# Kernel optimization log

Hardware: AMD Instinct MI355X
Metric: run time of the kernel (lower is better)

The kernel has to match this reference:

```python
import jax, jax.numpy as jnp
import numpy as np

B = 4
N_TOTAL = 40000
N_SRC0, N_DST0, E0 = 30000, 15000, 360000
N_DST1, E1 = 7500, 180000
D_IN, OUT = 64, 32
H1, C1 = 8, 8
H2, C2 = 1, OUT
NEG_SLOPE = 0.2


def setup_inputs() -> dict:
    key = jax.random.key(0)
    ks = jax.random.split(key, 16)
    inp = {
        'x': jax.random.normal(ks[0], (B, N_TOTAL, D_IN), dtype=jnp.float32),
        'n_id0': jax.random.randint(ks[1], (N_SRC0,), 0, N_SRC0),
        'res_n_id0': jax.random.randint(ks[2], (N_DST0,), 0, N_SRC0),
        'edge_src0': jax.random.randint(ks[3], (E0,), 0, N_SRC0),
        'edge_dst0': jax.random.randint(ks[4], (E0,), 0, N_DST0),
        'res_n_id1': jax.random.randint(ks[5], (N_DST1,), 0, N_DST0),
        'edge_src1': jax.random.randint(ks[6], (E1,), 0, N_DST0),
        'edge_dst1': jax.random.randint(ks[7], (E1,), 0, N_DST1),
        # GATConv params (Glorot-ish scale)
        'W1': jax.random.normal(ks[8], (D_IN, H1 * C1), dtype=jnp.float32) / np.sqrt(D_IN),
        'att_src1': jax.random.normal(ks[9], (H1, C1), dtype=jnp.float32) / np.sqrt(C1),
        'att_dst1': jax.random.normal(ks[10], (H1, C1), dtype=jnp.float32) / np.sqrt(C1),
        'b1': jnp.zeros((H1 * C1,), dtype=jnp.float32),
        'W2': jax.random.normal(ks[11], (H1 * C1, H2 * C2), dtype=jnp.float32) / np.sqrt(H1 * C1),
        'att_src2': jax.random.normal(ks[12], (H2, C2), dtype=jnp.float32) / np.sqrt(C2),
        'att_dst2': jax.random.normal(ks[13], (H2, C2), dtype=jnp.float32) / np.sqrt(C2),
        'b2': jnp.zeros((H2 * C2,), dtype=jnp.float32),
    }
    return inp


def gat_conv(x_src, x_dst, src, dst, W, a_src, a_dst, bias, n_dst, H, C):
    """Bipartite PyG-style GATConv (concat=True, eval mode, no self-loops)."""
    b = x_src.shape[0]
    hs = (x_src @ W).reshape(b, -1, H, C)            # [B, Ns, H, C]
    hd = (x_dst @ W).reshape(b, -1, H, C)            # [B, Nd, H, C]
    es = jnp.einsum('bnhc,hc->bnh', hs, a_src)       # [B, Ns, H]
    ed = jnp.einsum('bnhc,hc->bnh', hd, a_dst)       # [B, Nd, H]
    e = jax.nn.leaky_relu(es[:, src] + ed[:, dst], NEG_SLOPE)  # [B, E, H]
    eT = jnp.swapaxes(e, 0, 1)                       # [E, B, H] (segment over axis 0)
    m = jax.ops.segment_max(eT, dst, num_segments=n_dst)
    p = jnp.exp(eT - m[dst])
    den = jax.ops.segment_sum(p, dst, num_segments=n_dst)
    alpha = p / den[dst]                             # [E, B, H]
    msg = alpha[..., None] * jnp.swapaxes(hs[:, src], 0, 1)    # [E, B, H, C]
    out = jax.ops.segment_sum(msg, dst, num_segments=n_dst)    # [Nd, B, H, C]
    out = jnp.swapaxes(out, 0, 1).reshape(b, n_dst, H * C)
    return out + bias


def reference(x, n_id0, res_n_id0, edge_src0, edge_dst0, res_n_id1, edge_src1,
              edge_dst1, W1, att_src1, att_dst1, b1, W2, att_src2, att_dst2, b2):
    xt = x[:, n_id0, :]                                        # [B, N_SRC0, D_IN]
    h = gat_conv(xt, xt[:, res_n_id0, :], edge_src0, edge_dst0,
                 W1, att_src1, att_dst1, b1, N_DST0, H1, C1)
    h = jax.nn.elu(h)                                          # dropout = identity (eval)
    out = gat_conv(h, h[:, res_n_id1, :], edge_src1, edge_dst1,
                   W2, att_src2, att_dst2, b2, N_DST1, H2, C2)
    return out                                                 # [B, N_DST1, OUT]
```

## Files before the change

### kernel.cpp

```cpp
#include <hip/hip_runtime.h>

#define NB 4
#define NT 40000
#define NS0 30000
#define ND0 15000
#define NE0 360000
#define ND1 7500
#define NE1 180000
#define NEG 0.2f

#define CAP 64
#define K1B ((NB*NS0)/64)
#define SB4 ((NE0 + NE1 + 1023)/1024)

typedef __attribute__((ext_vector_type(8))) short bf8;
typedef __attribute__((ext_vector_type(4))) float f4;

__device__ __forceinline__ unsigned short f2bf(float f) {
    unsigned u = __float_as_uint(f);
    u += 0x7FFF + ((u >> 16) & 1);
    return (unsigned short)(u >> 16);
}
__device__ __forceinline__ float bf_lo(unsigned u) { return __uint_as_float(u << 16); }
__device__ __forceinline__ float bf_hi(unsigned u) { return __uint_as_float(u & 0xFFFF0000u); }

__global__ __launch_bounds__(256) void kA_gemm_scat(
        const float* __restrict__ x, const int* __restrict__ n_id0,
        const float* __restrict__ W1, const float* __restrict__ a_src,
        const float* __restrict__ a_dst,
        unsigned short* __restrict__ ht1b, float* __restrict__ es1, float* __restrict__ ed1,
        const int* __restrict__ esrc0, const int* __restrict__ edst0,
        const int* __restrict__ esrc1, const int* __restrict__ edst1,
        int* __restrict__ cur0, int* __restrict__ cur1,
        int* __restrict__ srcsort0, int* __restrict__ srcsort1) {
    __shared__ unsigned short xtb[64*72];
    __shared__ unsigned short wtb[64*72];
    __shared__ float asl[64], adl[64];
    if (blockIdx.x < SB4) {
        int base = blockIdx.x * 1024 + threadIdx.x;
        #pragma unroll
        for (int p = 0; p < 4; ++p) {
            int t = base + p * 256;
            if (t < NE0) {
                int d = edst0[t];
                int pos = atomicAdd(&cur0[d], 1);
                if (pos < CAP) srcsort0[d*CAP + pos] = esrc0[t];
            } else if (t < NE0 + NE1) {
                int e = t - NE0;
                int d = edst1[e];
                int pos = atomicAdd(&cur1[d], 1);
                if (pos < CAP) srcsort1[d*CAP + pos] = esrc1[e];
            }
        }
        return;
    }
    int bid = blockIdx.x - SB4;
    int t = threadIdx.x;
    {
        int k = t >> 2, nb = (t & 3) * 16;
        const float* wrow = &W1[k*64 + nb];
        #pragma unroll
        for (int j = 0; j < 16; j += 4) {
            float4 v = *(const float4*)&wrow[j];
            wtb[(nb+j+0)*72 + k] = f2bf(v.x);
            wtb[(nb+j+1)*72 + k] = f2bf(v.y);
            wtb[(nb+j+2)*72 + k] = f2bf(v.z);
            wtb[(nb+j+3)*72 + k] = f2bf(v.w);
        }
    }
    if (t < 64) { asl[t] = a_src[t]; adl[t] = a_dst[t]; }
    {
        int rr = t & 63;
        int q4 = t >> 6;
        int row_s = bid * 64 + rr;
        int bs = row_s / NS0;
        int ns = row_s - bs * NS0;
        const float* xrow = x + ((size_t)(bs * NT + n_id0[ns])) * 64;
        #pragma unroll
        for (int j = 0; j < 4; ++j) {
            int k = q4 * 16 + j * 4;
            float4 v = *(const float4*)&xrow[k];
            ushort4 u;
            u.x = f2bf(v.x); u.y = f2bf(v.y); u.z = f2bf(v.z); u.w = f2bf(v.w);
            *(ushort4*)&xtb[rr*72 + k] = u;
        }
    }
    __syncthreads();
    int w = t >> 6, lane = t & 63, quad = lane >> 4, cl = lane & 15;
    int arow = 16*w + cl;
    bf8 a0 = *(const bf8*)&xtb[arow*72 + quad*8];
    bf8 a1 = *(const bf8*)&xtb[arow*72 + 32 + quad*8];
    f4 acc[4];
    #pragma unroll
    for (int sub = 0; sub < 4; ++sub) {
        int n = sub*16 + cl;
        bf8 b0 = *(const bf8*)&wtb[n*72 + quad*8];
        bf8 b1 = *(const bf8*)&wtb[n*72 + 32 + quad*8];
        f4 c = {0.f, 0.f, 0.f, 0.f};
        c = __builtin_amdgcn_mfma_f32_16x16x32_bf16(a0, b0, c, 0, 0, 0);
        c = __builtin_amdgcn_mfma_f32_16x16x32_bf16(a1, b1, c, 0, 0, 0);
        acc[sub] = c;
    }
    int rbase = bid*64 + 16*w + quad*4;
    #pragma unroll
    for (int sub = 0; sub < 4; ++sub)
        #pragma unroll
        for (int r = 0; r < 4; ++r)
            ht1b[(size_t)(rbase + r)*64 + sub*16 + cl] = f2bf(acc[sub][r]);
    #pragma unroll
    for (int r = 0; r < 4; ++r) {
        #pragma unroll
        for (int sub = 0; sub < 4; ++sub) {
            int col = sub*16 + cl;
            float ps = acc[sub][r] * asl[col];
            float pd = acc[sub][r] * adl[col];
            ps += __shfl_xor(ps, 1); ps += __shfl_xor(ps, 2); ps += __shfl_xor(ps, 4);
            pd += __shfl_xor(pd, 1); pd += __shfl_xor(pd, 2); pd += __shfl_xor(pd, 4);
            if ((cl & 7) == 0) {
                int h = sub*2 + (cl >> 3);
                es1[(rbase + r)*8 + h] = ps;
                ed1[(rbase + r)*8 + h] = pd;
            }
        }
    }
}

__global__ __launch_bounds__(256) void k3_agg1_node2(
        const int* __restrict__ srcsort0, const int* __restrict__ cur0,
        const int* __restrict__ res0,
        const float* __restrict__ es1, const float* __restrict__ ed1,
        const unsigned short* __restrict__ ht1b, const float* __restrict__ b1,
        const float* __restrict__ W2, const float* __restrict__ a_src2,
        const float* __restrict__ a_dst2,
        float* __restrict__ ht2, float* __restrict__ es2, float* __restrict__ ed2) {
    __shared__ float W2l[64*32];
    __shared__ float as2[32], ad2[32];
    __shared__ float hsh[4][64];
    int t = threadIdx.x;
    for (int i = t; i < 512; i += 256)
        *(float4*)&W2l[i*4] = *(const float4*)&W2[i*4];
    if (t < 32) { as2[t] = a_src2[t]; ad2[t] = a_dst2[t]; }
    __syncthreads();
    int xcd = blockIdx.x & 7;
    int b = xcd >> 1;
    int chunk = (blockIdx.x >> 3) * 2 + (xcd & 1);
    int wv = t >> 6;
    int d = chunk * 4 + wv;
    int lane = t & 63;
    int grp = lane >> 3;
    int c = lane & 7;
    int dn = res0[d];
    float edv = ed1[(b*NS0 + dn)*8 + c];
    int start = d * CAP;
    int cnt = cur0[d];
    const float* esb = es1 + (size_t)b*NS0*8;
    const unsigned short* htb = ht1b + (size_t)b*NS0*64;
    float acc[8] = {};
    float wsum = 0.f;
    int i = grp;
    bool v0 = i      < cnt, v1 = i + 8  < cnt,
         v2 = i + 16 < cnt, v3 = i + 24 < cnt;
    int s0 = v0 ? srcsort0[start + i]      : 0;
    int s1 = v1 ? srcsort0[start + i + 8]  : 0;
    int s2 = v2 ? srcsort0[start + i + 16] : 0;
    int s3 = v3 ? srcsort0[start + i + 24] : 0;
    for (;;) {
        float e0 = esb[s0*8 + c], e1 = esb[s1*8 + c];
        float e2 = esb[s2*8 + c], e3 = esb[s3*8 + c];
        uint4 h0 = *(const uint4*)&htb[(size_t)s0*64 + c*8];
        uint4 h1 = *(const uint4*)&htb[(size_t)s1*64 + c*8];
        uint4 h2 = *(const uint4*)&htb[(size_t)s2*64 + c*8];
        uint4 h3 = *(const uint4*)&htb[(size_t)s3*64 + c*8];
        int ni = i + 32;
        bool nv0 = ni      < cnt, nv1 = ni + 8  < cnt,
             nv2 = ni + 16 < cnt, nv3 = ni + 24 < cnt;
        int t0 = nv0 ? srcsort0[start + ni]      : 0;
        int t1 = nv1 ? srcsort0[start + ni + 8]  : 0;
        int t2 = nv2 ? srcsort0[start + ni + 16] : 0;
        int t3 = nv3 ? srcsort0[start + ni + 24] : 0;
        e0 += edv; e1 += edv; e2 += edv; e3 += edv;
        e0 = e0 > 0.f ? e0 : NEG * e0;
        e1 = e1 > 0.f ? e1 : NEG * e1;
        e2 = e2 > 0.f ? e2 : NEG * e2;
        e3 = e3 > 0.f ? e3 : NEG * e3;
        float w0 = v0 ? __expf(e0) : 0.f;
        float w1 = v1 ? __expf(e1) : 0.f;
        float w2 = v2 ? __expf(e2) : 0.f;
        float w3 = v3 ? __expf(e3) : 0.f;
        acc[0] = fmaf(w0, bf_lo(h0.x), acc[0]); acc[1] = fmaf(w0, bf_hi(h0.x), acc[1]);
        acc[2] = fmaf(w0, bf_lo(h0.y), acc[2]); acc[3] = fmaf(w0, bf_hi(h0.y), acc[3]);
        acc[4] = fmaf(w0, bf_lo(h0.z), acc[4]); acc[5] = fmaf(w0, bf_hi(h0.z), acc[5]);
        acc[6] = fmaf(w0, bf_lo(h0.w), acc[6]); acc[7] = fmaf(w0, bf_hi(h0.w), acc[7]);
        acc[0] = fmaf(w1, bf_lo(h1.x), acc[0]); acc[1] = fmaf(w1, bf_hi(h1.x), acc[1]);
        acc[2] = fmaf(w1, bf_lo(h1.y), acc[2]); acc[3] = fmaf(w1, bf_hi(h1.y), acc[3]);
        acc[4] = fmaf(w1, bf_lo(h1.z), acc[4]); acc[5] = fmaf(w1, bf_hi(h1.z), acc[5]);
        acc[6] = fmaf(w1, bf_lo(h1.w), acc[6]); acc[7] = fmaf(w1, bf_hi(h1.w), acc[7]);
        acc[0] = fmaf(w2, bf_lo(h2.x), acc[0]); acc[1] = fmaf(w2, bf_hi(h2.x), acc[1]);
        acc[2] = fmaf(w2, bf_lo(h2.y), acc[2]); acc[3] = fmaf(w2, bf_hi(h2.y), acc[3]);
        acc[4] = fmaf(w2, bf_lo(h2.z), acc[4]); acc[5] = fmaf(w2, bf_hi(h2.z), acc[5]);
        acc[6] = fmaf(w2, bf_lo(h2.w), acc[6]); acc[7] = fmaf(w2, bf_hi(h2.w), acc[7]);
        acc[0] = fmaf(w3, bf_lo(h3.x), acc[0]); acc[1] = fmaf(w3, bf_hi(h3.x), acc[1]);
        acc[2] = fmaf(w3, bf_lo(h3.y), acc[2]); acc[3] = fmaf(w3, bf_hi(h3.y), acc[3]);
        acc[4] = fmaf(w3, bf_lo(h3.z), acc[4]); acc[5] = fmaf(w3, bf_hi(h3.z), acc[5]);
        acc[6] = fmaf(w3, bf_lo(h3.w), acc[6]); acc[7] = fmaf(w3, bf_hi(h3.w), acc[7]);
        wsum += (w0 + w1) + (w2 + w3);
        i = ni; s0 = t0; s1 = t1; s2 = t2; s3 = t3;
        v0 = nv0; v1 = nv1; v2 = nv2; v3 = nv3;
        if (i >= cnt) break;
    }
    #pragma unroll
    for (int j = 0; j < 8; ++j) {
        acc[j] += __shfl_xor(acc[j], 8);
        acc[j] += __shfl_xor(acc[j], 16);
        acc[j] += __shfl_xor(acc[j], 32);
    }
    wsum += __shfl_xor(wsum, 8); wsum += __shfl_xor(wsum, 16); wsum += __shfl_xor(wsum, 32);
    if (grp == 0) {
        float inv = cnt > 0 ? 1.f / wsum : 0.f;
        float4 b_lo = *(const float4*)&b1[c*8];
        float4 b_hi = *(const float4*)&b1[c*8 + 4];
        float o[8];
        o[0] = acc[0]*inv + b_lo.x; o[1] = acc[1]*inv + b_lo.y;
        o[2] = acc[2]*inv + b_lo.z; o[3] = acc[3]*inv + b_lo.w;
        o[4] = acc[4]*inv + b_hi.x; o[5] = acc[5]*inv + b_hi.y;
        o[6] = acc[6]*inv + b_hi.z; o[7] = acc[7]*inv + b_hi.w;
        #pragma unroll
        for (int j = 0; j < 8; ++j) o[j] = o[j] > 0.f ? o[j] : __expf(o[j]) - 1.f;
        float* hrow = &hsh[wv][c*8];
        *(float4*)&hrow[0] = make_float4(o[0], o[1], o[2], o[3]);
        *(float4*)&hrow[4] = make_float4(o[4], o[5], o[6], o[7]);
    }
    int c2 = lane & 31, half = lane >> 5;
    float acc2 = 0.f;
    #pragma unroll
    for (int k = 0; k < 32; ++k)
        acc2 = fmaf(hsh[wv][half*32 + k], W2l[(half*32 + k)*32 + c2], acc2);
    acc2 += __shfl_xor(acc2, 32);
    float ps = acc2 * as2[c2];
    float pd = acc2 * ad2[c2];
    ps += __shfl_xor(ps, 1); ps += __shfl_xor(ps, 2); ps += __shfl_xor(ps, 4);
    ps += __shfl_xor(ps, 8); ps += __shfl_xor(ps, 16);
    pd += __shfl_xor(pd, 1); pd += __shfl_xor(pd, 2); pd += __shfl_xor(pd, 4);
    pd += __shfl_xor(pd, 8); pd += __shfl_xor(pd, 16);
    int row = b*ND0 + d;
    if (half == 0) ht2[(size_t)row*32 + c2] = acc2;
    if (lane == 0) { es2[row] = ps; ed2[row] = pd; }
}

__global__ __launch_bounds__(256) void k7_agg2(
        const int* __restrict__ srcsort1, const int* __restrict__ cur1,
        const int* __restrict__ res1,
        const float* __restrict__ es2, const float* __restrict__ ed2,
        const float* __restrict__ ht2, const float* __restrict__ b2,
        float* __restrict__ outp) {
    int xcd = blockIdx.x & 7;
    int b = xcd >> 1;
    int chunk = (blockIdx.x >> 3) * 2 + (xcd & 1);
    if (chunk >= ND1/4) return;
    int d = chunk * 4 + (threadIdx.x >> 6);
    int lane = threadIdx.x & 63;
    int grp = lane >> 3;
    int c = lane & 7;
    int dn = res1[d];
    float edv = ed2[b*ND0 + dn];
    int start = d * CAP;
    int cnt = cur1[d];
    const float* esb = es2 + (size_t)b*ND0;
    const float* htb = ht2 + (size_t)b*ND0*32;
    float ax = 0.f, ay = 0.f, az = 0.f, aw = 0.f, wsum = 0.f;
    int i = grp;
    bool v0 = i      < cnt, v1 = i + 8  < cnt,
         v2 = i + 16 < cnt, v3 = i + 24 < cnt;
    int s0 = v0 ? srcsort1[start + i]      : 0;
    int s1 = v1 ? srcsort1[start + i + 8]  : 0;
    int s2 = v2 ? srcsort1[start + i + 16] : 0;
    int s3 = v3 ? srcsort1[start + i + 24] : 0;
    for (;;) {
        float lg0 = esb[s0], lg1 = esb[s1], lg2 = esb[s2], lg3 = esb[s3];
        float4 h0 = *(const float4*)&htb[(size_t)s0*32 + c*4];
        float4 h1 = *(const float4*)&htb[(size_t)s1*32 + c*4];
        float4 h2 = *(const float4*)&htb[(size_t)s2*32 + c*4];
        float4 h3 = *(const float4*)&htb[(size_t)s3*32 + c*4];
        int ni = i + 32;
        bool nv0 = ni      < cnt, nv1 = ni + 8  < cnt,
             nv2 = ni + 16 < cnt, nv3 = ni + 24 < cnt;
        int t0 = nv0 ? srcsort1[start + ni]      : 0;
        int t1 = nv1 ? srcsort1[start + ni + 8]  : 0;
        int t2 = nv2 ? srcsort1[start + ni + 16] : 0;
        int t3 = nv3 ? srcsort1[start + ni + 24] : 0;
        lg0 += edv; lg1 += edv; lg2 += edv; lg3 += edv;
        lg0 = lg0 > 0.f ? lg0 : NEG * lg0;
        lg1 = lg1 > 0.f ? lg1 : NEG * lg1;
        lg2 = lg2 > 0.f ? lg2 : NEG * lg2;
        lg3 = lg3 > 0.f ? lg3 : NEG * lg3;
        float w0 = v0 ? __expf(lg0) : 0.f;
        float w1 = v1 ? __expf(lg1) : 0.f;
        float w2 = v2 ? __expf(lg2) : 0.f;
        float w3 = v3 ? __expf(lg3) : 0.f;
        ax = fmaf(w0, h0.x, ax); ay = fmaf(w0, h0.y, ay);
        az = fmaf(w0, h0.z, az); aw = fmaf(w0, h0.w, aw);
        ax = fmaf(w1, h1.x, ax); ay = fmaf(w1, h1.y, ay);
        az = fmaf(w1, h1.z, az); aw = fmaf(w1, h1.w, aw);
        ax = fmaf(w2, h2.x, ax); ay = fmaf(w2, h2.y, ay);
        az = fmaf(w2, h2.z, az); aw = fmaf(w2, h2.w, aw);
        ax = fmaf(w3, h3.x, ax); ay = fmaf(w3, h3.y, ay);
        az = fmaf(w3, h3.z, az); aw = fmaf(w3, h3.w, aw);
        wsum += (w0 + w1) + (w2 + w3);
        i = ni; s0 = t0; s1 = t1; s2 = t2; s3 = t3;
        v0 = nv0; v1 = nv1; v2 = nv2; v3 = nv3;
        if (i >= cnt) break;
    }
    ax += __shfl_xor(ax, 8); ax += __shfl_xor(ax, 16); ax += __shfl_xor(ax, 32);
    ay += __shfl_xor(ay, 8); ay += __shfl_xor(ay, 16); ay += __shfl_xor(ay, 32);
    az += __shfl_xor(az, 8); az += __shfl_xor(az, 16); az += __shfl_xor(az, 32);
    aw += __shfl_xor(aw, 8); aw += __shfl_xor(aw, 16); aw += __shfl_xor(aw, 32);
    wsum += __shfl_xor(wsum, 8); wsum += __shfl_xor(wsum, 16); wsum += __shfl_xor(wsum, 32);
    if (grp == 0) {
        float inv = cnt > 0 ? 1.f / wsum : 0.f;
        float4 bb = *(const float4*)&b2[c*4];
        float4 o;
        o.x = ax*inv + bb.x; o.y = ay*inv + bb.y;
        o.z = az*inv + bb.z; o.w = aw*inv + bb.w;
        *(float4*)&outp[((size_t)(b*ND1 + d))*32 + c*4] = o;
    }
}

extern "C" void kernel_launch(void* const* d_in, const int* in_sizes, int n_in,
                              void* d_out, int out_size, void* d_ws, size_t ws_size,
                              hipStream_t stream) {
    const float* x        = (const float*)d_in[0];
    const int*   n_id0    = (const int*)d_in[1];
    const int*   res0     = (const int*)d_in[2];
    const int*   esrc0    = (const int*)d_in[3];
    const int*   edst0    = (const int*)d_in[4];
    const int*   res1     = (const int*)d_in[5];
    const int*   esrc1    = (const int*)d_in[6];
    const int*   edst1    = (const int*)d_in[7];
    const float* W1       = (const float*)d_in[8];
    const float* a_src1   = (const float*)d_in[9];
    const float* a_dst1   = (const float*)d_in[10];
    const float* b1       = (const float*)d_in[11];
    const float* W2       = (const float*)d_in[12];
    const float* a_src2   = (const float*)d_in[13];
    const float* a_dst2   = (const float*)d_in[14];
    const float* b2       = (const float*)d_in[15];
    float* outp = (float*)d_out;

    char* base = (char*)d_ws;
    unsigned short* ht1b = (unsigned short*)base;
    float* es1  = (float*)(base + 15360000);
    float* ed1  = es1 + 960000;
    float* ht2  = ed1 + 960000;
    float* es2  = ht2 + 1920000;
    float* ed2  = es2 + 60000;
    int* cur0     = (int*)(ed2 + 60000);
    int* cur1     = cur0 + ND0;
    int* srcsort0 = cur1 + ND1;
    int* srcsort1 = srcsort0 + ND0*CAP;

    hipMemsetAsync(cur0, 0, (ND0 + ND1) * sizeof(int), stream);
    kA_gemm_scat<<<K1B + SB4, 256, 0, stream>>>(x, n_id0, W1, a_src1, a_dst1,
                                                ht1b, es1, ed1,
                                                esrc0, edst0, esrc1, edst1,
                                                cur0, cur1, srcsort0, srcsort1);
    k3_agg1_node2<<<NB*(ND0/4), 256, 0, stream>>>(srcsort0, cur0, res0, es1, ed1, ht1b, b1,
                                                  W2, a_src2, a_dst2, ht2, es2, ed2);
    k7_agg2<<<7504, 256, 0, stream>>>(srcsort1, cur1, res1, es2, ed2, ht2, b2, outp);
}
```

Baseline: 204.2 us.

## Retune edge-scatter blocks, transpose-reduce aggregation, vectorize W2 matvec, guard index prefetch

```diff
diff --git a/kernel.cpp b/kernel.cpp
--- a/kernel.cpp
+++ b/kernel.cpp
@@ -11,7 +11,7 @@
 
 #define CAP 64
 #define K1B ((NB*NS0)/64)
-#define SB4 ((NE0 + NE1 + 1023)/1024)
+#define HB  ((NE0 + NE1 + 255)/256)
 
 typedef __attribute__((ext_vector_type(8))) short bf8;
 typedef __attribute__((ext_vector_type(4))) float f4;
@@ -36,25 +36,21 @@
     __shared__ unsigned short xtb[64*72];
     __shared__ unsigned short wtb[64*72];
     __shared__ float asl[64], adl[64];
-    if (blockIdx.x < SB4) {
-        int base = blockIdx.x * 1024 + threadIdx.x;
-        #pragma unroll
-        for (int p = 0; p < 4; ++p) {
-            int t = base + p * 256;
-            if (t < NE0) {
-                int d = edst0[t];
-                int pos = atomicAdd(&cur0[d], 1);
-                if (pos < CAP) srcsort0[d*CAP + pos] = esrc0[t];
-            } else if (t < NE0 + NE1) {
-                int e = t - NE0;
-                int d = edst1[e];
-                int pos = atomicAdd(&cur1[d], 1);
-                if (pos < CAP) srcsort1[d*CAP + pos] = esrc1[e];
-            }
+    if (blockIdx.x >= K1B) {
+        int t = (blockIdx.x - K1B) * 256 + threadIdx.x;
+        if (t < NE0) {
+            int d = edst0[t];
+            int pos = atomicAdd(&cur0[d], 1);
+            if (pos < CAP) srcsort0[d*CAP + pos] = esrc0[t];
+        } else if (t < NE0 + NE1) {
+            int e = t - NE0;
+            int d = edst1[e];
+            int pos = atomicAdd(&cur1[d], 1);
+            if (pos < CAP) srcsort1[d*CAP + pos] = esrc1[e];
         }
         return;
     }
-    int bid = blockIdx.x - SB4;
+    int bid = blockIdx.x;
     int t = threadIdx.x;
     {
         int k = t >> 2, nb = (t & 3) * 16;
@@ -95,10 +91,10 @@
     for (int sub = 0; sub < 4; ++sub) {
         int n = sub*16 + cl;
         bf8 b0 = *(const bf8*)&wtb[n*72 + quad*8];
-        bf8 b1 = *(const bf8*)&wtb[n*72 + 32 + quad*8];
+        bf8 b1v = *(const bf8*)&wtb[n*72 + 32 + quad*8];
         f4 c = {0.f, 0.f, 0.f, 0.f};
         c = __builtin_amdgcn_mfma_f32_16x16x32_bf16(a0, b0, c, 0, 0, 0);
-        c = __builtin_amdgcn_mfma_f32_16x16x32_bf16(a1, b1, c, 0, 0, 0);
+        c = __builtin_amdgcn_mfma_f32_16x16x32_bf16(a1, b1v, c, 0, 0, 0);
         acc[sub] = c;
     }
     int rbase = bid*64 + 16*w + quad*4;
@@ -133,13 +129,20 @@
         const float* __restrict__ W2, const float* __restrict__ a_src2,
         const float* __restrict__ a_dst2,
         float* __restrict__ ht2, float* __restrict__ es2, float* __restrict__ ed2) {
-    __shared__ float W2l[64*32];
+    __shared__ float W2t[32][68];
     __shared__ float as2[32], ad2[32];
+    __shared__ float b1l[64];
     __shared__ float hsh[4][64];
     int t = threadIdx.x;
-    for (int i = t; i < 512; i += 256)
-        *(float4*)&W2l[i*4] = *(const float4*)&W2[i*4];
+    {
+        float4 v0 = *(const float4*)&W2[t*8];
+        float4 v1 = *(const float4*)&W2[t*8 + 4];
+        int k = t >> 2, c = (t & 3) * 8;
+        W2t[c+0][k] = v0.x; W2t[c+1][k] = v0.y; W2t[c+2][k] = v0.z; W2t[c+3][k] = v0.w;
+        W2t[c+4][k] = v1.x; W2t[c+5][k] = v1.y; W2t[c+6][k] = v1.z; W2t[c+7][k] = v1.w;
+    }
     if (t < 32) { as2[t] = a_src2[t]; ad2[t] = a_dst2[t]; }
+    if (t < 64) b1l[t] = b1[t];
     __syncthreads();
     int xcd = blockIdx.x & 7;
     int b = xcd >> 1;
@@ -172,12 +175,16 @@
         uint4 h2 = *(const uint4*)&htb[(size_t)s2*64 + c*8];
         uint4 h3 = *(const uint4*)&htb[(size_t)s3*64 + c*8];
         int ni = i + 32;
-        bool nv0 = ni      < cnt, nv1 = ni + 8  < cnt,
-             nv2 = ni + 16 < cnt, nv3 = ni + 24 < cnt;
-        int t0 = nv0 ? srcsort0[start + ni]      : 0;
-        int t1 = nv1 ? srcsort0[start + ni + 8]  : 0;
-        int t2 = nv2 ? srcsort0[start + ni + 16] : 0;
-        int t3 = nv3 ? srcsort0[start + ni + 24] : 0;
+        bool nv0 = false, nv1 = false, nv2 = false, nv3 = false;
+        int t0 = 0, t1 = 0, t2 = 0, t3 = 0;
+        if (ni < cnt) {
+            nv0 = true;            nv1 = ni + 8  < cnt;
+            nv2 = ni + 16 < cnt;   nv3 = ni + 24 < cnt;
+            t0 =       srcsort0[start + ni];
+            t1 = nv1 ? srcsort0[start + ni + 8]  : 0;
+            t2 = nv2 ? srcsort0[start + ni + 16] : 0;
+            t3 = nv3 ? srcsort0[start + ni + 24] : 0;
+        }
         e0 += edv; e1 += edv; e2 += edv; e3 += edv;
         e0 = e0 > 0.f ? e0 : NEG * e0;
         e1 = e1 > 0.f ? e1 : NEG * e1;
@@ -208,33 +215,41 @@
         v0 = nv0; v1 = nv1; v2 = nv2; v3 = nv3;
         if (i >= cnt) break;
     }
-    #pragma unroll
-    for (int j = 0; j < 8; ++j) {
-        acc[j] += __shfl_xor(acc[j], 8);
-        acc[j] += __shfl_xor(acc[j], 16);
-        acc[j] += __shfl_xor(acc[j], 32);
+    int g0 = grp & 1, g1 = (grp >> 1) & 1, g2 = grp >> 2;
+    float n0, n1, n2, n3;
+    {
+        float s, r;
+        s = g0 ? acc[0] : acc[1]; r = __shfl_xor(s, 8);  n0 = (g0 ? acc[1] : acc[0]) + r;
+        s = g0 ? acc[2] : acc[3]; r = __shfl_xor(s, 8);  n1 = (g0 ? acc[3] : acc[2]) + r;
+        s = g0 ? acc[4] : acc[5]; r = __shfl_xor(s, 8);  n2 = (g0 ? acc[5] : acc[4]) + r;
+        s = g0 ? acc[6] : acc[7]; r = __shfl_xor(s, 8);  n3 = (g0 ? acc[7] : acc[6]) + r;
+    }
+    float m0, m1;
+    {
+        float s, r;
+        s = g1 ? n0 : n1; r = __shfl_xor(s, 16); m0 = (g1 ? n1 : n0) + r;
+        s = g1 ? n2 : n3; r = __shfl_xor(s, 16); m1 = (g1 ? n3 : n2) + r;
+    }
+    float fin;
+    {
+        float s = g2 ? m0 : m1; float r = __shfl_xor(s, 32); fin = (g2 ? m1 : m0) + r;
     }
     wsum += __shfl_xor(wsum, 8); wsum += __shfl_xor(wsum, 16); wsum += __shfl_xor(wsum, 32);
-    if (grp == 0) {
-        float inv = cnt > 0 ? 1.f / wsum : 0.f;
-        float4 b_lo = *(const float4*)&b1[c*8];
-        float4 b_hi = *(const float4*)&b1[c*8 + 4];
-        float o[8];
-        o[0] = acc[0]*inv + b_lo.x; o[1] = acc[1]*inv + b_lo.y;
-        o[2] = acc[2]*inv + b_lo.z; o[3] = acc[3]*inv + b_lo.w;
-        o[4] = acc[4]*inv + b_hi.x; o[5] = acc[5]*inv + b_hi.y;
-        o[6] = acc[6]*inv + b_hi.z; o[7] = acc[7]*inv + b_hi.w;
-        #pragma unroll
-        for (int j = 0; j < 8; ++j) o[j] = o[j] > 0.f ? o[j] : __expf(o[j]) - 1.f;
-        float* hrow = &hsh[wv][c*8];
-        *(float4*)&hrow[0] = make_float4(o[0], o[1], o[2], o[3]);
-        *(float4*)&hrow[4] = make_float4(o[4], o[5], o[6], o[7]);
-    }
+    float inv = cnt > 0 ? 1.f / wsum : 0.f;
+    float o = fin * inv + b1l[(c << 3) | grp];
+    o = o > 0.f ? o : __expf(o) - 1.f;
+    hsh[wv][(c << 3) | grp] = o;
     int c2 = lane & 31, half = lane >> 5;
+    const float4* hp = (const float4*)&hsh[wv][half * 32];
+    const float4* wp = (const float4*)&W2t[c2][half * 32];
     float acc2 = 0.f;
     #pragma unroll
-    for (int k = 0; k < 32; ++k)
-        acc2 = fmaf(hsh[wv][half*32 + k], W2l[(half*32 + k)*32 + c2], acc2);
+    for (int q = 0; q < 8; ++q) {
+        float4 hv = hp[q];
+        float4 w4 = wp[q];
+        acc2 = fmaf(hv.x, w4.x, acc2); acc2 = fmaf(hv.y, w4.y, acc2);
+        acc2 = fmaf(hv.z, w4.z, acc2); acc2 = fmaf(hv.w, w4.w, acc2);
+    }
     acc2 += __shfl_xor(acc2, 32);
     float ps = acc2 * as2[c2];
     float pd = acc2 * ad2[c2];
@@ -282,12 +297,16 @@
         float4 h2 = *(const float4*)&htb[(size_t)s2*32 + c*4];
         float4 h3 = *(const float4*)&htb[(size_t)s3*32 + c*4];
         int ni = i + 32;
-        bool nv0 = ni      < cnt, nv1 = ni + 8  < cnt,
-             nv2 = ni + 16 < cnt, nv3 = ni + 24 < cnt;
-        int t0 = nv0 ? srcsort1[start + ni]      : 0;
-        int t1 = nv1 ? srcsort1[start + ni + 8]  : 0;
-        int t2 = nv2 ? srcsort1[start + ni + 16] : 0;
-        int t3 = nv3 ? srcsort1[start + ni + 24] : 0;
+        bool nv0 = false, nv1 = false, nv2 = false, nv3 = false;
+        int t0 = 0, t1 = 0, t2 = 0, t3 = 0;
+        if (ni < cnt) {
+            nv0 = true;            nv1 = ni + 8  < cnt;
+            nv2 = ni + 16 < cnt;   nv3 = ni + 24 < cnt;
+            t0 =       srcsort1[start + ni];
+            t1 = nv1 ? srcsort1[start + ni + 8]  : 0;
+            t2 = nv2 ? srcsort1[start + ni + 16] : 0;
+            t3 = nv3 ? srcsort1[start + ni + 24] : 0;
+        }
         lg0 += edv; lg1 += edv; lg2 += edv; lg3 += edv;
         lg0 = lg0 > 0.f ? lg0 : NEG * lg0;
         lg1 = lg1 > 0.f ? lg1 : NEG * lg1;
@@ -359,10 +378,10 @@
     int* srcsort1 = srcsort0 + ND0*CAP;
 
     hipMemsetAsync(cur0, 0, (ND0 + ND1) * sizeof(int), stream);
-    kA_gemm_scat<<<K1B + SB4, 256, 0, stream>>>(x, n_id0, W1, a_src1, a_dst1,
-                                                ht1b, es1, ed1,
-                                                esrc0, edst0, esrc1, edst1,
-                                                cur0, cur1, srcsort0, srcsort1);
+    kA_gemm_scat<<<K1B + HB, 256, 0, stream>>>(x, n_id0, W1, a_src1, a_dst1,
+                                               ht1b, es1, ed1,
+                                               esrc0, edst0, esrc1, edst1,
+                                               cur0, cur1, srcsort0, srcsort1);
     k3_agg1_node2<<<NB*(ND0/4), 256, 0, stream>>>(srcsort0, cur0, res0, es1, ed1, ht1b, b1,
                                                   W2, a_src2, a_dst2, ht2, es2, ed2);
     k7_agg2<<<7504, 256, 0, stream>>>(srcsort1, cur1, res1, es2, ed2, ht2, b2, outp);
```

New measurement: 196.9 us. 1.04x faster.
